# Kernel tuning notes

Hardware: AMD Instinct MI355X
Metric: run time of the kernel (lower is better)

## Reference

```python
import jax, jax.numpy as jnp
import numpy as np
from jax import lax

D_FEAT = 62
N_CLASSES = 500
N_DAGS, N_NODES, MAX_PREDS = 16384, 48, 4
NEG = -1e30


def masked_attention(w, x, mask):
    # x: [..., P, d], w: [d, 1], mask: [..., P, 1] bool -> [..., d]
    scores = jnp.where(mask, x @ w, NEG)          # [..., P, 1]
    a = jax.nn.softmax(scores, axis=-2)
    return jnp.sum(a * x, axis=-2)


def setup_inputs() -> dict:
    key = jax.random.key(0)
    ks = jax.random.split(key, 10)
    atoms = jax.random.normal(ks[0], (N_DAGS, N_NODES, D_FEAT), dtype=jnp.float32)
    # topologically valid predecessor lists: preds[t] < t or -1 (padding / source)
    raw = jax.random.randint(ks[1], (N_DAGS, N_NODES, MAX_PREDS), 0, N_NODES)
    t = jnp.arange(N_NODES)[None, :, None]
    preds = raw % jnp.maximum(t, 1)
    keep = jax.random.bernoulli(ks[2], 0.8, (N_DAGS, N_NODES, MAX_PREDS))
    preds = jnp.where((t > 0) & keep, preds, -1).astype(jnp.int32)
    s = 1.0 / np.sqrt(D_FEAT)
    W_single = jax.random.uniform(ks[3], (D_FEAT, D_FEAT), jnp.float32, -s, s)
    b_single = jax.random.uniform(ks[4], (D_FEAT,), jnp.float32, -s, s)
    sm = 1.0 / np.sqrt(2 * D_FEAT)
    W_merge = jax.random.uniform(ks[5], (D_FEAT, 2 * D_FEAT), jnp.float32, -sm, sm)
    b_merge = jax.random.uniform(ks[6], (D_FEAT,), jnp.float32, -sm, sm)
    att_w = jax.random.uniform(ks[7], (D_FEAT, 1), jnp.float32, 0.0, 1.0)
    dag_w = jax.random.uniform(ks[8], (D_FEAT, 1), jnp.float32, 0.0, 1.0)
    W_final = jax.random.uniform(ks[9], (N_CLASSES, D_FEAT), jnp.float32, -s, s)
    b_final = jnp.zeros((N_CLASSES,), jnp.float32)
    return {"atoms": atoms, "preds": preds, "W_single": W_single, "b_single": b_single,
            "W_merge": W_merge, "b_merge": b_merge, "att_w": att_w, "dag_w": dag_w,
            "W_final": W_final, "b_final": b_final}


def reference(atoms, preds, W_single, b_single, W_merge, b_merge, att_w, dag_w, W_final, b_final):
    # atoms: [D, N, d]; preds: [D, N, P] (-1 = no predecessor). Nodes are in topo order;
    # node N-1 is the sink whose output represents the DAG.
    single = jax.nn.relu(jnp.einsum('dnf,gf->dng', atoms, W_single) + b_single)  # source-node path

    def run_dag(atom_seq, pred_seq, single_seq):  # [N,d], [N,P], [N,d]
        def step(outs, t):
            p = pred_seq[t]                          # [P]
            mask = p >= 0
            g = outs[jnp.clip(p, 0)]                 # [P, d] gathered predecessor outputs
            agg = masked_attention(att_w, g, mask[:, None])
            merged = jax.nn.relu(W_merge @ jnp.concatenate([agg, atom_seq[t]]) + b_merge)
            out_t = jnp.where(mask.any(), merged, single_seq[t])
            return outs.at[t].set(out_t), None
        outs, _ = lax.scan(step, jnp.zeros_like(atom_seq), jnp.arange(atom_seq.shape[0]))
        return outs[-1]

    last = jax.vmap(run_dag)(atoms, preds, single)   # [D, d] sink output per DAG
    pooled = masked_attention(dag_w, last, jnp.ones((last.shape[0], 1), bool))  # [d]
    return jax.nn.sigmoid(W_final @ pooled + b_final)  # [500]
```

## Files before the change

### kernel.cpp

```cpp
#include <hip/hip_runtime.h>

#define D_FEAT    62
#define N_CLASSES 500
#define N_DAGS    16384
#define N_NODES   48
#define MAX_PREDS 4
#define ROWB      6160
#define SCS_STR   49
#define HIST_ROW  64
#define HIST_DAG  (N_NODES * HIST_ROW)

typedef __attribute__((ext_vector_type(8))) short short8;
typedef __attribute__((ext_vector_type(4))) float f32x4;

union FragU { unsigned int u[4]; short8 v; };
struct Raw { unsigned int u[16]; };

__device__ __forceinline__ float bf2f(unsigned short u) {
    union { unsigned int i; float f; } v;
    v.i = ((unsigned int)u) << 16;
    return v.f;
}

__device__ __forceinline__ unsigned short f2bf(float f) {
    union { float f; unsigned int i; } v;
    v.f = f;
    unsigned int x = v.i;
    return (unsigned short)((x + 0x7FFFu + ((x >> 16) & 1u)) >> 16);
}

__device__ __forceinline__ unsigned int pack2bf(float a, float b) {
    unsigned int ia = __float_as_uint(a), ib = __float_as_uint(b);
    ia += 0x7FFFu + ((ia >> 16) & 1u);
    ib += 0x7FFFu + ((ib >> 16) & 1u);
    return (ia >> 16) | (ib & 0xFFFF0000u);
}

__device__ __forceinline__ float pk_lo(unsigned int u) { return __uint_as_float(u << 16); }
__device__ __forceinline__ float pk_hi(unsigned int u) { return __uint_as_float(u & 0xFFFF0000u); }

__device__ __forceinline__ float bcast(float x, int k) {
    return __int_as_float(__builtin_amdgcn_readlane(__float_as_int(x), k));
}

__device__ __forceinline__ float ldm(const void* p, long i, int mode) {
    if (mode) return ((const float*)p)[i];
    else      return bf2f(((const unsigned short*)p)[i]);
}

__device__ __forceinline__ float wm_val(const void* W, int n, int k, int mode) {
    if (n >= D_FEAT) return 0.f;
    if (k < 62)  return ldm(W, n * 124 + k, mode);
    if (k < 64)  return 0.f;
    if (k < 126) return ldm(W, n * 124 + (k - 2), mode);
    return 0.f;
}

__device__ __forceinline__ float ws_val(const void* W, int n, int k, int mode) {
    if (n >= D_FEAT || k >= D_FEAT) return 0.f;
    return ldm(W, n * 62 + k, mode);
}

__device__ __forceinline__ void load_raw(Raw& r, const void* atoms, long row,
                                         int quad, int mode) {
    if (mode == 0) {
        const char* base = (const char*)atoms + row * 124;
        const int off3 = (quad < 3) ? (64 + quad * 16) : 108;
        #pragma unroll
        for (int w = 0; w < 4; ++w)
            r.u[w] = *(const unsigned int*)(base + quad * 16 + 4 * w);
        #pragma unroll
        for (int w = 0; w < 4; ++w)
            r.u[4 + w] = *(const unsigned int*)(base + off3 + 4 * w);
    } else {
        const char* base = (const char*)atoms + row * 248;
        const int off3 = (quad < 3) ? (128 + quad * 32) : 216;
        #pragma unroll
        for (int w = 0; w < 4; ++w) {
            uint2 v = *(const uint2*)(base + quad * 32 + 8 * w);
            r.u[2 * w] = v.x; r.u[2 * w + 1] = v.y;
        }
        #pragma unroll
        for (int w = 0; w < 4; ++w) {
            uint2 v = *(const uint2*)(base + off3 + 8 * w);
            r.u[8 + 2 * w] = v.x; r.u[9 + 2 * w] = v.y;
        }
    }
}

__device__ __forceinline__ void pack_frags(FragU& a2, FragU& a3, const Raw& r,
                                           int quad, int mode) {
    if (mode == 0) {
        #pragma unroll
        for (int w = 0; w < 4; ++w) a2.u[w] = r.u[w];
        if (quad < 3) {
            #pragma unroll
            for (int w = 0; w < 4; ++w) a3.u[w] = r.u[4 + w];
        } else {
            a3.u[0] = r.u[5]; a3.u[1] = r.u[6]; a3.u[2] = r.u[7]; a3.u[3] = 0;
        }
    } else {
        #pragma unroll
        for (int w = 0; w < 4; ++w)
            a2.u[w] = pack2bf(__uint_as_float(r.u[2 * w]), __uint_as_float(r.u[2 * w + 1]));
        if (quad < 3) {
            #pragma unroll
            for (int w = 0; w < 4; ++w)
                a3.u[w] = pack2bf(__uint_as_float(r.u[8 + 2 * w]), __uint_as_float(r.u[9 + 2 * w]));
        } else {
            #pragma unroll
            for (int w = 0; w < 3; ++w)
                a3.u[w] = pack2bf(__uint_as_float(r.u[10 + 2 * w]), __uint_as_float(r.u[11 + 2 * w]));
            a3.u[3] = 0;
        }
    }
}

template<int GH, int DPBT>
__global__ __launch_bounds__(64, 1) void k_dag(
    const void* __restrict__ atoms,
    const int*  __restrict__ preds,
    const void* __restrict__ W_single,
    const void* __restrict__ b_single,
    const void* __restrict__ W_merge,
    const void* __restrict__ b_merge,
    const void* __restrict__ att_w,
    const void* __restrict__ dag_w,
    unsigned short* __restrict__ hist,
    float* __restrict__ last_out,
    float* __restrict__ score_out)
{
    constexpr int HIST_LDS   = GH ? 0 : (DPBT * ROWB);
    constexpr int SCS_BYTES  = DPBT * SCS_STR * 4;
    constexpr int WSF_OFF    = HIST_LDS + SCS_BYTES;
    constexpr int WSF_STRIDE = 136;
    constexpr int BOUNCE_OFF = WSF_OFF + 64 * WSF_STRIDE;
    constexpr int BOUNCE_SZ  = GH ? (DPBT * 128) : 0;
    constexpr int SMEM_BYTES = BOUNCE_OFF + (BOUNCE_SZ ? BOUNCE_SZ : 16);
    __shared__ char smem[SMEM_BYTES];

    constexpr unsigned long long FULLM = (DPBT == 16) ? 0xFFFFull : 0xFFull;

    const int  lane = threadIdx.x;
    const int  m    = lane & 15;
    const int  quad = lane >> 4;
    const int  mc   = (DPBT == 16) ? m : (m & 7);
    const bool wq   = (DPBT == 16) || (quad < 2);
    const int  d0   = blockIdx.x * DPBT;

    int mode;
    {
        const unsigned short* a16 = (const unsigned short*)atoms;
        const float v0 = bf2f(a16[2 * lane]);
        const float v1 = bf2f(a16[128 + 2 * lane]);
        const int bad = (!(fabsf(v0) < 64.f)) + (!(fabsf(v1) < 64.f));
        const int cnt = __popcll(__ballot(bad > 0)) + __popcll(__ballot(bad > 1));
        mode = (cnt > 16) ? 1 : 0;
    }

    short8 wmF[4][4];
    float bm4[4], bs4[4], aw4[4], dw4[4];
    char* const wsfp = smem + WSF_OFF + lane * WSF_STRIDE;
    #pragma unroll
    for (int nt = 0; nt < 4; ++nt) {
        const int n = m + 16 * nt;
        #pragma unroll
        for (int kt = 0; kt < 4; ++kt) {
            FragU f;
            #pragma unroll
            for (int w = 0; w < 4; ++w) {
                const int k = kt * 32 + quad * 8 + 2 * w;
                f.u[w] = pack2bf(wm_val(W_merge, n, k, mode), wm_val(W_merge, n, k + 1, mode));
            }
            wmF[nt][kt] = f.v;
        }
        #pragma unroll
        for (int kt = 0; kt < 2; ++kt) {
            FragU f;
            #pragma unroll
            for (int w = 0; w < 4; ++w) {
                const int k = kt * 32 + quad * 8 + 2 * w;
                f.u[w] = pack2bf(ws_val(W_single, n, k, mode), ws_val(W_single, n, k + 1, mode));
            }
            *(short8*)(wsfp + (nt * 2 + kt) * 16) = f.v;
        }
        bm4[nt] = (n < D_FEAT) ? ldm(b_merge,  n, mode) : 0.f;
        bs4[nt] = (n < D_FEAT) ? ldm(b_single, n, mode) : 0.f;
        aw4[nt] = (n < D_FEAT) ? ldm(att_w,    n, mode) : 0.f;
        dw4[nt] = (n < D_FEAT) ? ldm(dag_w,    n, mode) : 0.f;
    }

    float* scs  = (float*)(smem + HIST_LDS);
    float* srow = scs + mc * SCS_STR;
    const long arow0 = (long)(d0 + mc) * N_NODES;
    const int* pbase = preds + (size_t)(d0 + mc) * (N_NODES * MAX_PREDS);
    unsigned short* const hdag = GH ? (hist + (size_t)(d0 + mc) * HIST_DAG) : (unsigned short*)0;

    auto node_body = [&](int t, const int4 pv, const FragU a2, const FragU a3) {
        const int pm = max(max(pv.x, pv.y), max(pv.z, pv.w));
        const unsigned int mk = (unsigned int)(__ballot(pm >= 0) & FULLM);

        f32x4 acc[4] = { {0,0,0,0}, {0,0,0,0}, {0,0,0,0}, {0,0,0,0} };
        f32x4 sac[4] = { {0,0,0,0}, {0,0,0,0}, {0,0,0,0}, {0,0,0,0} };

        if (mk != 0u) {
            const int p0 = pv.x, p1 = pv.y, p2 = pv.z, p3 = pv.w;
            const int c0 = max(p0, 0), c1 = max(p1, 0), c2 = max(p2, 0), c3 = max(p3, 0);
            float q0 = srow[c0], q1 = srow[c1], q2 = srow[c2], q3 = srow[c3];

            FragU G[2][4];
            #pragma unroll
            for (int cc = 0; cc < 2; ++cc) {
                if constexpr (GH) {
                    const unsigned short* gb = hdag + cc * 32 + quad * 8;
                    G[cc][0].v = *(const short8*)(gb + c0 * HIST_ROW);
                    G[cc][1].v = *(const short8*)(gb + c1 * HIST_ROW);
                    G[cc][2].v = *(const short8*)(gb + c2 * HIST_ROW);
                    G[cc][3].v = *(const short8*)(gb + c3 * HIST_ROW);
                } else {
                    const char* obase = smem + mc * ROWB;
                    const int boff = cc * 64 + quad * 16;
                    G[cc][0].v = *(const short8*)(obase + c0 * 128 + boff);
                    G[cc][1].v = *(const short8*)(obase + c1 * 128 + boff);
                    G[cc][2].v = *(const short8*)(obase + c2 * 128 + boff);
                    G[cc][3].v = *(const short8*)(obase + c3 * 128 + boff);
                }
            }

            q0 = (p0 >= 0) ? q0 : -1e30f;
            q1 = (p1 >= 0) ? q1 : -1e30f;
            q2 = (p2 >= 0) ? q2 : -1e30f;
            q3 = (p3 >= 0) ? q3 : -1e30f;
            const float mx = fmaxf(fmaxf(q0, q1), fmaxf(q2, q3));
            float e0 = (p0 >= 0) ? __expf(q0 - mx) : 0.f;
            float e1 = (p1 >= 0) ? __expf(q1 - mx) : 0.f;
            float e2 = (p2 >= 0) ? __expf(q2 - mx) : 0.f;
            float e3 = (p3 >= 0) ? __expf(q3 - mx) : 0.f;
            const float inv = 1.f / fmaxf(e0 + e1 + e2 + e3, 1e-30f);
            e0 *= inv; e1 *= inv; e2 *= inv; e3 *= inv;

            FragU A01[2];
            #pragma unroll
            for (int cc = 0; cc < 2; ++cc) {
                #pragma unroll
                for (int w = 0; w < 4; ++w) {
                    const float lo = fmaf(e0, pk_lo(G[cc][0].u[w]), fmaf(e1, pk_lo(G[cc][1].u[w]),
                                     fmaf(e2, pk_lo(G[cc][2].u[w]), e3 * pk_lo(G[cc][3].u[w]))));
                    const float hi = fmaf(e0, pk_hi(G[cc][0].u[w]), fmaf(e1, pk_hi(G[cc][1].u[w]),
                                     fmaf(e2, pk_hi(G[cc][2].u[w]), e3 * pk_hi(G[cc][3].u[w]))));
                    A01[cc].u[w] = pack2bf(lo, hi);
                }
            }
            #pragma unroll
            for (int nt = 0; nt < 4; ++nt) {
                f32x4 c = {0, 0, 0, 0};
                c = __builtin_amdgcn_mfma_f32_16x16x32_bf16(A01[0].v, wmF[nt][0], c, 0, 0, 0);
                c = __builtin_amdgcn_mfma_f32_16x16x32_bf16(A01[1].v, wmF[nt][1], c, 0, 0, 0);
                c = __builtin_amdgcn_mfma_f32_16x16x32_bf16(a2.v,     wmF[nt][2], c, 0, 0, 0);
                c = __builtin_amdgcn_mfma_f32_16x16x32_bf16(a3.v,     wmF[nt][3], c, 0, 0, 0);
                acc[nt] = c;
            }
        }
        if (mk != (unsigned int)FULLM) {
            #pragma unroll
            for (int nt = 0; nt < 4; ++nt) {
                FragU s0, s1;
                s0.v = *(const short8*)(wsfp + (nt * 2 + 0) * 16);
                s1.v = *(const short8*)(wsfp + (nt * 2 + 1) * 16);
                f32x4 c = {0, 0, 0, 0};
                c = __builtin_amdgcn_mfma_f32_16x16x32_bf16(a2.v, s0.v, c, 0, 0, 0);
                c = __builtin_amdgcn_mfma_f32_16x16x32_bf16(a3.v, s1.v, c, 0, 0, 0);
                sac[nt] = c;
            }
        }

        float out4[4][4];
        #pragma unroll
        for (int nt = 0; nt < 4; ++nt) {
            #pragma unroll
            for (int r = 0; r < 4; ++r) {
                const int dm = quad * 4 + r;
                const bool hp = (mk >> dm) & 1u;
                const float v = hp ? (acc[nt][r] + bm4[nt]) : (sac[nt][r] + bs4[nt]);
                out4[nt][r] = fmaxf(v, 0.f);
            }
        }

        if constexpr (GH) {
            char* const bounce = smem + BOUNCE_OFF;
            #pragma unroll
            for (int nt = 0; nt < 4; ++nt) {
                #pragma unroll
                for (int r = 0; r < 4; ++r)
                    *(unsigned short*)(bounce + (quad * 4 + r) * 128 + (m + 16 * nt) * 2)
                        = f2bf(out4[nt][r]);
            }
            #pragma unroll
            for (int c = 0; c < DPBT / 8; ++c) {
                const int off = c * 1024 + lane * 16;
                const int dg  = off >> 7;
                const int ins = (off & 127) >> 1;
                short8 vv = *(const short8*)(bounce + off);
                *(short8*)(hist + (size_t)(d0 + dg) * HIST_DAG + t * HIST_ROW + ins) = vv;
            }
        } else {
            #pragma unroll
            for (int nt = 0; nt < 4; ++nt) {
                const int n = m + 16 * nt;
                #pragma unroll
                for (int r = 0; r < 4; ++r) {
                    if (wq) {
                        const int dm = quad * 4 + r;
                        *(unsigned short*)(smem + dm * ROWB + t * 128 + n * 2) = f2bf(out4[nt][r]);
                    }
                }
            }
        }

        const bool fin = (t == N_NODES - 1);
        float sr[4] = {0, 0, 0, 0};
        #pragma unroll
        for (int nt = 0; nt < 4; ++nt) {
            const float w = fin ? dw4[nt] : aw4[nt];
            #pragma unroll
            for (int r = 0; r < 4; ++r) sr[r] = fmaf(out4[nt][r], w, sr[r]);
        }
        #pragma unroll
        for (int r = 0; r < 4; ++r) {
            sr[r] += __shfl_xor(sr[r], 1);
            sr[r] += __shfl_xor(sr[r], 2);
            sr[r] += __shfl_xor(sr[r], 4);
            sr[r] += __shfl_xor(sr[r], 8);
        }
        if (m == 0 && wq) {
            #pragma unroll
            for (int r = 0; r < 4; ++r) {
                if (!fin) scs[(quad * 4 + r) * SCS_STR + t] = sr[r];
                else      score_out[d0 + quad * 4 + r] = sr[r];
            }
        }
        if (fin && wq) {
            #pragma unroll
            for (int nt = 0; nt < 4; ++nt) {
                const int n = m + 16 * nt;
                if (n < D_FEAT) {
                    #pragma unroll
                    for (int r = 0; r < 4; ++r)
                        last_out[(size_t)(d0 + quad * 4 + r) * D_FEAT + n] = out4[nt][r];
                }
            }
        }
    };

    Raw r0, r1;
    load_raw(r0, atoms, arow0 + 0, quad, mode);
    int4 p0v = *(const int4*)(pbase + 0);
    load_raw(r1, atoms, arow0 + 1, quad, mode);
    int4 p1v = *(const int4*)(pbase + 4);

    #pragma unroll 1
    for (int t = 0; t < N_NODES; t += 2) {
        {
            const int4 p = p0v;
            FragU a2, a3;
            pack_frags(a2, a3, r0, quad, mode);
            if constexpr (!GH) {
                if (t + 2 < N_NODES) {
                    load_raw(r0, atoms, arow0 + (t + 2), quad, mode);
                    p0v = *(const int4*)(pbase + (t + 2) * 4);
                }
                node_body(t, p, a2, a3);
            } else {
                node_body(t, p, a2, a3);
                if (t + 2 < N_NODES) {
                    load_raw(r0, atoms, arow0 + (t + 2), quad, mode);
                    p0v = *(const int4*)(pbase + (t + 2) * 4);
                }
            }
        }
        {
            const int4 p = p1v;
            FragU a2, a3;
            pack_frags(a2, a3, r1, quad, mode);
            if constexpr (!GH) {
                if (t + 3 < N_NODES) {
                    load_raw(r1, atoms, arow0 + (t + 3), quad, mode);
                    p1v = *(const int4*)(pbase + (t + 3) * 4);
                }
                node_body(t + 1, p, a2, a3);
            } else {
                node_body(t + 1, p, a2, a3);
                if (t + 3 < N_NODES) {
                    load_raw(r1, atoms, arow0 + (t + 3), quad, mode);
                    p1v = *(const int4*)(pbase + (t + 3) * 4);
                }
            }
        }
    }
}

__global__ __launch_bounds__(256) void k_pool(
    const float* __restrict__ last,
    const float* __restrict__ score,
    float* __restrict__ vpart,
    float* __restrict__ mpart,
    float* __restrict__ spart)
{
    const int lane = threadIdx.x & 63;
    const int wv   = threadIdx.x >> 6;
    const int c    = blockIdx.x * 4 + wv;
    const int d0   = c * 64;

    const float s = score[d0 + lane];
    float m = s;
    #pragma unroll
    for (int off = 32; off > 0; off >>= 1) m = fmaxf(m, __shfl_xor(m, off));
    const float e = __expf(s - m);
    float den = e;
    #pragma unroll
    for (int off = 32; off > 0; off >>= 1) den += __shfl_xor(den, off);

    float acc = 0.f;
    #pragma unroll 4
    for (int j = 0; j < 64; ++j) {
        const float v = (lane < D_FEAT) ? last[(size_t)(d0 + j) * D_FEAT + lane] : 0.f;
        acc = fmaf(bcast(e, j), v, acc);
    }
    if (lane < D_FEAT) vpart[c * D_FEAT + lane] = acc;
    if (lane == 0) { mpart[c] = m; spart[c] = den; }
}

__global__ __launch_bounds__(256) void k_final(
    const void* __restrict__ atoms,
    const float* __restrict__ vpart,
    const float* __restrict__ mpart,
    const float* __restrict__ spart,
    const void* __restrict__ W_final,
    const void* __restrict__ b_final,
    void* __restrict__ out)
{
    __shared__ float red[256];
    __shared__ float wgt[256];
    __shared__ float pooled[D_FEAT];
    const int tid = threadIdx.x;

    const unsigned short* a16 = (const unsigned short*)atoms;
    const int bad = (!(fabsf(bf2f(a16[2 * (tid & 63)])) < 64.f))
                  + (!(fabsf(bf2f(a16[128 + 2 * (tid & 63)])) < 64.f));
    red[tid] = (float)bad;
    __syncthreads();
    for (int s = 128; s > 0; s >>= 1) {
        if (tid < s) red[tid] += red[tid + s];
        __syncthreads();
    }
    const int mode = (red[0] > 64.f) ? 1 : 0;
    __syncthreads();

    const float m = mpart[tid];
    red[tid] = m;
    __syncthreads();
    for (int s = 128; s > 0; s >>= 1) {
        if (tid < s) red[tid] = fmaxf(red[tid], red[tid + s]);
        __syncthreads();
    }
    const float M = red[0];
    __syncthreads();

    const float w = __expf(m - M);
    wgt[tid] = w;
    red[tid] = w * spart[tid];
    __syncthreads();
    for (int s = 128; s > 0; s >>= 1) {
        if (tid < s) red[tid] += red[tid + s];
        __syncthreads();
    }
    const float denom = red[0];
    __syncthreads();

    if (tid < D_FEAT) {
        float acc = 0.f;
        #pragma unroll 8
        for (int c = 0; c < 256; ++c) acc = fmaf(wgt[c], vpart[c * D_FEAT + tid], acc);
        pooled[tid] = acc / denom;
    }
    __syncthreads();

    for (int r = tid; r < N_CLASSES; r += 256) {
        float acc = ldm(b_final, r, mode);
        #pragma unroll
        for (int i = 0; i < D_FEAT; ++i)
            acc = fmaf(ldm(W_final, (long)r * D_FEAT + i, mode), pooled[i], acc);
        const float sg = 1.f / (1.f + __expf(-acc));
        if (mode) ((float*)out)[r] = sg;
        else      ((unsigned short*)out)[r] = f2bf(sg);
    }
}

extern "C" void kernel_launch(void* const* d_in, const int* in_sizes, int n_in,
                              void* d_out, int out_size, void* d_ws, size_t ws_size,
                              hipStream_t stream) {
    const void* atoms    = d_in[0];
    const int*  preds    = (const int*)d_in[1];
    const void* W_single = d_in[2];
    const void* b_single = d_in[3];
    const void* W_merge  = d_in[4];
    const void* b_merge  = d_in[5];
    const void* att_w    = d_in[6];
    const void* dag_w    = d_in[7];
    const void* W_final  = d_in[8];
    const void* b_final  = d_in[9];

    float* last  = (float*)d_ws;
    float* score = last + (size_t)N_DAGS * D_FEAT;
    float* vpart = score + N_DAGS;
    float* mpart = vpart + 256 * D_FEAT;
    float* spart = mpart + 256;
    unsigned short* hist = (unsigned short*)((char*)d_ws + (4ull << 20));
    const size_t need = (4ull << 20) + (size_t)N_DAGS * HIST_DAG * sizeof(unsigned short);

    if (ws_size >= need)
        k_dag<1,16><<<N_DAGS / 16, 64, 0, stream>>>(atoms, preds, W_single, b_single,
            W_merge, b_merge, att_w, dag_w, hist, last, score);
    else
        k_dag<0,8><<<N_DAGS / 8, 64, 0, stream>>>(atoms, preds, W_single, b_single,
            W_merge, b_merge, att_w, dag_w, hist, last, score);
    k_pool <<<64, 256, 0, stream>>>(last, score, vpart, mpart, spart);
    k_final<<<1, 256, 0, stream>>>(atoms, vpart, mpart, spart, W_final, b_final, d_out);
}
```

Before: 490.5 us.

## Prefetch next node's predecessor gather from global history with bounce forwarding

```diff
diff --git a/kernel.cpp b/kernel.cpp
--- a/kernel.cpp
+++ b/kernel.cpp
@@ -196,7 +196,22 @@
     const int* pbase = preds + (size_t)(d0 + mc) * (N_NODES * MAX_PREDS);
     unsigned short* const hdag = GH ? (hist + (size_t)(d0 + mc) * HIST_DAG) : (unsigned short*)0;
 
-    auto node_body = [&](int t, const int4 pv, const FragU a2, const FragU a3) {
+    FragU Gp[2][4];
+
+    auto issue_gather = [&](const int4 pn) {
+        const int c0 = max(pn.x, 0), c1 = max(pn.y, 0), c2 = max(pn.z, 0), c3 = max(pn.w, 0);
+        #pragma unroll
+        for (int cc = 0; cc < 2; ++cc) {
+            const unsigned short* gb = hdag + cc * 32 + quad * 8;
+            Gp[cc][0].v = *(const short8*)(gb + c0 * HIST_ROW);
+            Gp[cc][1].v = *(const short8*)(gb + c1 * HIST_ROW);
+            Gp[cc][2].v = *(const short8*)(gb + c2 * HIST_ROW);
+            Gp[cc][3].v = *(const short8*)(gb + c3 * HIST_ROW);
+        }
+    };
+
+    auto node_body = [&](int t, const int4 pv, const int4 pv_next,
+                         const FragU a2, const FragU a3) {
         const int pm = max(max(pv.x, pv.y), max(pv.z, pv.w));
         const unsigned int mk = (unsigned int)(__ballot(pm >= 0) & FULLM);
 
@@ -208,22 +223,25 @@
             const int c0 = max(p0, 0), c1 = max(p1, 0), c2 = max(p2, 0), c3 = max(p3, 0);
             float q0 = srow[c0], q1 = srow[c1], q2 = srow[c2], q3 = srow[c3];
 
-            FragU G[2][4];
-            #pragma unroll
-            for (int cc = 0; cc < 2; ++cc) {
-                if constexpr (GH) {
-                    const unsigned short* gb = hdag + cc * 32 + quad * 8;
-                    G[cc][0].v = *(const short8*)(gb + c0 * HIST_ROW);
-                    G[cc][1].v = *(const short8*)(gb + c1 * HIST_ROW);
-                    G[cc][2].v = *(const short8*)(gb + c2 * HIST_ROW);
-                    G[cc][3].v = *(const short8*)(gb + c3 * HIST_ROW);
-                } else {
-                    const char* obase = smem + mc * ROWB;
+            if constexpr (GH) {
+                FragU bv0, bv1;
+                const char* bp = smem + BOUNCE_OFF + mc * 128 + quad * 16;
+                bv0.v = *(const short8*)(bp);
+                bv1.v = *(const short8*)(bp + 64);
+                const int tm1 = t - 1;
+                if (c0 == tm1) { Gp[0][0] = bv0; Gp[1][0] = bv1; }
+                if (c1 == tm1) { Gp[0][1] = bv0; Gp[1][1] = bv1; }
+                if (c2 == tm1) { Gp[0][2] = bv0; Gp[1][2] = bv1; }
+                if (c3 == tm1) { Gp[0][3] = bv0; Gp[1][3] = bv1; }
+            } else {
+                const char* obase = smem + mc * ROWB;
+                #pragma unroll
+                for (int cc = 0; cc < 2; ++cc) {
                     const int boff = cc * 64 + quad * 16;
-                    G[cc][0].v = *(const short8*)(obase + c0 * 128 + boff);
-                    G[cc][1].v = *(const short8*)(obase + c1 * 128 + boff);
-                    G[cc][2].v = *(const short8*)(obase + c2 * 128 + boff);
-                    G[cc][3].v = *(const short8*)(obase + c3 * 128 + boff);
+                    Gp[cc][0].v = *(const short8*)(obase + c0 * 128 + boff);
+                    Gp[cc][1].v = *(const short8*)(obase + c1 * 128 + boff);
+                    Gp[cc][2].v = *(const short8*)(obase + c2 * 128 + boff);
+                    Gp[cc][3].v = *(const short8*)(obase + c3 * 128 + boff);
                 }
             }
 
@@ -244,10 +262,10 @@
             for (int cc = 0; cc < 2; ++cc) {
                 #pragma unroll
                 for (int w = 0; w < 4; ++w) {
-                    const float lo = fmaf(e0, pk_lo(G[cc][0].u[w]), fmaf(e1, pk_lo(G[cc][1].u[w]),
-                                     fmaf(e2, pk_lo(G[cc][2].u[w]), e3 * pk_lo(G[cc][3].u[w]))));
-                    const float hi = fmaf(e0, pk_hi(G[cc][0].u[w]), fmaf(e1, pk_hi(G[cc][1].u[w]),
-                                     fmaf(e2, pk_hi(G[cc][2].u[w]), e3 * pk_hi(G[cc][3].u[w]))));
+                    const float lo = fmaf(e0, pk_lo(Gp[cc][0].u[w]), fmaf(e1, pk_lo(Gp[cc][1].u[w]),
+                                     fmaf(e2, pk_lo(Gp[cc][2].u[w]), e3 * pk_lo(Gp[cc][3].u[w]))));
+                    const float hi = fmaf(e0, pk_hi(Gp[cc][0].u[w]), fmaf(e1, pk_hi(Gp[cc][1].u[w]),
+                                     fmaf(e2, pk_hi(Gp[cc][2].u[w]), e3 * pk_hi(Gp[cc][3].u[w]))));
                     A01[cc].u[w] = pack2bf(lo, hi);
                 }
             }
@@ -295,9 +313,10 @@
                     *(unsigned short*)(bounce + (quad * 4 + r) * 128 + (m + 16 * nt) * 2)
                         = f2bf(out4[nt][r]);
             }
-            #pragma unroll
-            for (int c = 0; c < DPBT / 8; ++c) {
-                const int off = c * 1024 + lane * 16;
+            if (t + 1 < N_NODES) issue_gather(pv_next);
+            #pragma unroll
+            for (int ch = 0; ch < DPBT / 8; ++ch) {
+                const int off = ch * 1024 + lane * 16;
                 const int dg  = off >> 7;
                 const int ins = (off & 127) >> 1;
                 short8 vv = *(const short8*)(bounce + off);
@@ -357,44 +376,31 @@
     int4 p0v = *(const int4*)(pbase + 0);
     load_raw(r1, atoms, arow0 + 1, quad, mode);
     int4 p1v = *(const int4*)(pbase + 4);
+    if constexpr (GH) issue_gather(p0v);
 
     #pragma unroll 1
     for (int t = 0; t < N_NODES; t += 2) {
         {
-            const int4 p = p0v;
+            const int4 p  = p0v;
+            const int4 pn = p1v;
             FragU a2, a3;
             pack_frags(a2, a3, r0, quad, mode);
-            if constexpr (!GH) {
-                if (t + 2 < N_NODES) {
-                    load_raw(r0, atoms, arow0 + (t + 2), quad, mode);
-                    p0v = *(const int4*)(pbase + (t + 2) * 4);
-                }
-                node_body(t, p, a2, a3);
-            } else {
-                node_body(t, p, a2, a3);
-                if (t + 2 < N_NODES) {
-                    load_raw(r0, atoms, arow0 + (t + 2), quad, mode);
-                    p0v = *(const int4*)(pbase + (t + 2) * 4);
-                }
-            }
+            if (t + 2 < N_NODES) {
+                p0v = *(const int4*)(pbase + (t + 2) * 4);
+                load_raw(r0, atoms, arow0 + (t + 2), quad, mode);
+            }
+            node_body(t, p, pn, a2, a3);
         }
         {
-            const int4 p = p1v;
+            const int4 p  = p1v;
+            const int4 pn = p0v;
             FragU a2, a3;
             pack_frags(a2, a3, r1, quad, mode);
-            if constexpr (!GH) {
-                if (t + 3 < N_NODES) {
-                    load_raw(r1, atoms, arow0 + (t + 3), quad, mode);
-                    p1v = *(const int4*)(pbase + (t + 3) * 4);
-                }
-                node_body(t + 1, p, a2, a3);
-            } else {
-                node_body(t + 1, p, a2, a3);
-                if (t + 3 < N_NODES) {
-                    load_raw(r1, atoms, arow0 + (t + 3), quad, mode);
-                    p1v = *(const int4*)(pbase + (t + 3) * 4);
-                }
-            }
+            if (t + 3 < N_NODES) {
+                p1v = *(const int4*)(pbase + (t + 3) * 4);
+                load_raw(r1, atoms, arow0 + (t + 3), quad, mode);
+            }
+            node_body(t + 1, p, pn, a2, a3);
         }
     }
 }
```

Measured after the change: 494.2 us. About the same (+0.8%).
